# Optimization experiments

Hardware: AMD Instinct MI355X
Metric: run time of the kernel (lower is better)

Reference implementation:

```python
import jax, jax.numpy as jnp
import numpy as np

E, R, CIN, COUT = 8, 8, 256, 256
B, H, W = 16, 64, 64
DN = ('NCHW', 'OIHW', 'NCHW')


def setup_inputs() -> dict:
    key = jax.random.key(0)
    k1, k2, k3, k4 = jax.random.split(key, 4)
    x = jax.random.normal(k1, (B, CIN, H, W), jnp.float32)
    probs = jax.nn.softmax(jax.random.normal(k2, (E,), jnp.float32))
    # in conv: rank filters over in_channels, kernel (1,3); out conv: kernel (3,1)
    weight_in = jax.random.normal(k3, (E, R, CIN, 1, 3), jnp.float32) * 0.02
    weight_out = jax.random.normal(k4, (E, COUT, R, 3, 1), jnp.float32) * 0.02
    return {"x": x, "probs": probs, "weight_in": weight_in, "weight_out": weight_out}


def _expert_conv(x, w_in, w_out):
    # in conv: stride (1,1), padding (0,1) -> [B,R,H,W]
    h = jax.lax.conv_general_dilated(x, w_in, window_strides=(1, 1),
                                     padding=[(0, 0), (1, 1)], dimension_numbers=DN)
    # out conv: stride (1,1), padding (1,0) -> [B,COUT,H,W]
    return jax.lax.conv_general_dilated(h, w_out, window_strides=(1, 1),
                                        padding=[(1, 1), (0, 0)], dimension_numbers=DN)


def reference(x, probs, weight_in, weight_out):
    # vmap over experts replaces the Python loop; outs: [E,B,COUT,H,W]
    outs = jax.vmap(lambda wi, wo: _expert_conv(x, wi, wo))(weight_in, weight_out)
    # probability-weighted sum over experts (stack + sum in the original)
    return jnp.einsum('e,ebchw->bchw', probs, outs)
```

## Files before the change

### kernel.cpp

```cpp
#include <hip/hip_runtime.h>
#include <hip/hip_bf16.h>


typedef __bf16 bf16x8 __attribute__((ext_vector_type(8)));
typedef __bf16 bf16x4 __attribute__((ext_vector_type(4)));
typedef float  f32x4  __attribute__((ext_vector_type(4)));

#define CIN_  256
#define COUT_ 256
#define M1    64
#define K1    768
#define K2    192
#define CS    264
#define HS2   264

static __device__ __forceinline__ unsigned short f2bf(float f) {
    union { float f; unsigned u; } v; v.f = f;
    unsigned r = v.u + 0x7FFFu + ((v.u >> 16) & 1u);
    return (unsigned short)(r >> 16);
}

__global__ void prep_weights(const float* __restrict__ probs,
                             const float* __restrict__ w_in,
                             const float* __restrict__ w_out,
                             unsigned short* __restrict__ W1,
                             unsigned short* __restrict__ W2) {
    int idx = blockIdx.x * blockDim.x + threadIdx.x;
    if (idx < M1 * K1) {
        int er = idx / K1, rem = idx % K1;
        int kx = rem / CIN_, c = rem % CIN_;
        int e = er >> 3;
        W1[idx] = f2bf(probs[e] * w_in[(er * CIN_ + c) * 3 + kx]);
    } else {
        int i2 = idx - M1 * K1;
        int o = i2 / K2, rem = i2 % K2;
        int ky = rem / M1, er = rem % M1;
        int e = er >> 3, r = er & 7;
        W2[i2] = f2bf(w_out[((e * COUT_ + o) * 8 + r) * 3 + ky]);
    }
}

__global__ __launch_bounds__(256, 2)
void fused_kernel(const float* __restrict__ x,
                  const unsigned short* __restrict__ W1,
                  const unsigned short* __restrict__ W2,
                  float* __restrict__ out) {
    __shared__ unsigned short xs[66 * CS];
    __shared__ unsigned short hs[64 * HS2];
    const int bid  = blockIdx.x;
    const int b    = (bid & 7) + ((bid >> 8) << 3);
    const int s    = (bid >> 3) & 31;
    const int y0   = s << 1;
    const int tid  = threadIdx.x;
    const int lane = tid & 63;
    const int wave = tid >> 6;
    const int g    = lane >> 4;
    const int lr   = lane & 15;

    bf16x8 w1f[3][8];
    {
        const unsigned short* w1p = W1 + (wave * 16 + lr) * K1 + g * 8;
        #pragma unroll
        for (int kx = 0; kx < 3; ++kx)
            #pragma unroll
            for (int cc = 0; cc < 8; ++cc)
                w1f[kx][cc] = *(const bf16x8*)(w1p + kx * CIN_ + cc * 32);
    }

    if (tid < 66) {
        int row = (tid < 33) ? 0 : 65;
        int col = (tid - (tid < 33 ? 0 : 33)) * 8;
        bf16x4 z4 = {};
        *(bf16x4*)&xs[row * CS + col] = z4;
        *(bf16x4*)&xs[row * CS + col + 4] = z4;
    }

    const int crow = tid >> 4;
    const int n4   = (tid & 15) << 2;
    const int swzt = (tid & 7) << 3;

    for (int yy = 0; yy < 4; ++yy) {
        const int y = y0 - 1 + yy;
        const bool yok = ((unsigned)y < 64u);
        __syncthreads();
        const float* xbase = x + ((b * CIN_ + crow) * 64 + (yok ? y : 0)) * 64 + n4;
        unsigned short* wr = &xs[(n4 + 1) * CS];
        #pragma unroll
        for (int r = 0; r < 4; ++r) {
            float4 ld[4];
            if (yok) {
                #pragma unroll
                for (int q = 0; q < 4; ++q)
                    ld[q] = *(const float4*)(xbase + (r * 4 + q) * 16 * 4096);
            } else {
                #pragma unroll
                for (int q = 0; q < 4; ++q) ld[q] = make_float4(0.f, 0.f, 0.f, 0.f);
            }
            #pragma unroll
            for (int q = 0; q < 4; ++q) {
                int cx = ((r * 4 + q) * 16 + crow) ^ swzt;
                *(__bf16*)&wr[0 * CS + cx] = (__bf16)ld[q].x;
                *(__bf16*)&wr[1 * CS + cx] = (__bf16)ld[q].y;
                *(__bf16*)&wr[2 * CS + cx] = (__bf16)ld[q].z;
                *(__bf16*)&wr[3 * CS + cx] = (__bf16)ld[q].w;
            }
        }
        __syncthreads();

        f32x4 acc[4];
        #pragma unroll
        for (int i = 0; i < 4; ++i) acc[i] = (f32x4){0.f, 0.f, 0.f, 0.f};
        #pragma unroll
        for (int kx = 0; kx < 3; ++kx) {
            int ns0 = lr + kx;
            int sz0 = (((ns0 - 1) >> 2) & 7) << 3;
            int ns1 = ns0 + 16, sz1 = (((ns1 - 1) >> 2) & 7) << 3;
            int ns2 = ns0 + 32, sz2 = (((ns2 - 1) >> 2) & 7) << 3;
            int ns3 = ns0 + 48, sz3 = (((ns3 - 1) >> 2) & 7) << 3;
            const unsigned short* r0  = &xs[ns0 * CS];
            const unsigned short* r1  = &xs[ns1 * CS];
            const unsigned short* r2p = &xs[ns2 * CS];
            const unsigned short* r3  = &xs[ns3 * CS];
            #pragma unroll
            for (int cc = 0; cc < 8; ++cc) {
                int co = cc * 32 + g * 8;
                acc[0] = __builtin_amdgcn_mfma_f32_16x16x32_bf16(
                    w1f[kx][cc], *(const bf16x8*)&r0[co ^ sz0], acc[0], 0, 0, 0);
                acc[1] = __builtin_amdgcn_mfma_f32_16x16x32_bf16(
                    w1f[kx][cc], *(const bf16x8*)&r1[co ^ sz1], acc[1], 0, 0, 0);
                acc[2] = __builtin_amdgcn_mfma_f32_16x16x32_bf16(
                    w1f[kx][cc], *(const bf16x8*)&r2p[co ^ sz2], acc[2], 0, 0, 0);
                acc[3] = __builtin_amdgcn_mfma_f32_16x16x32_bf16(
                    w1f[kx][cc], *(const bf16x8*)&r3[co ^ sz3], acc[3], 0, 0, 0);
            }
        }
        #pragma unroll
        for (int nt = 0; nt < 4; ++nt) {
            int n = nt * 16 + lr;
            bf16x4 pk;
            #pragma unroll
            for (int r2 = 0; r2 < 4; ++r2) pk[r2] = (__bf16)acc[nt][r2];
            int col = (yy * 64 + wave * 16 + g * 4) ^ ((n & 7) << 3);
            *(bf16x4*)&hs[n * HS2 + col] = pk;
        }
    }
    __syncthreads();

    bf16x8 w2f[4][6];
    #pragma unroll
    for (int ot = 0; ot < 4; ++ot)
        #pragma unroll
        for (int kc = 0; kc < 6; ++kc)
            w2f[ot][kc] = *(const bf16x8*)(W2 + ((wave * 4 + ot) * 16 + lr) * K2 +
                                           kc * 32 + g * 8);

    #pragma unroll
    for (int ry = 0; ry < 2; ++ry) {
        f32x4 acc2[4][4];
        #pragma unroll
        for (int ot = 0; ot < 4; ++ot)
            #pragma unroll
            for (int nt = 0; nt < 4; ++nt) acc2[ot][nt] = (f32x4){0.f, 0.f, 0.f, 0.f};

        #pragma unroll
        for (int kc = 0; kc < 6; ++kc) {
            bf16x8 bfrag[4];
            #pragma unroll
            for (int nt = 0; nt < 4; ++nt) {
                int n = nt * 16 + lr;
                int col = (ry * 64 + kc * 32 + g * 8) ^ ((n & 7) << 3);
                bfrag[nt] = *(const bf16x8*)&hs[n * HS2 + col];
            }
            #pragma unroll
            for (int ot = 0; ot < 4; ++ot)
                #pragma unroll
                for (int nt = 0; nt < 4; ++nt)
                    acc2[ot][nt] = __builtin_amdgcn_mfma_f32_16x16x32_bf16(
                        w2f[ot][kc], bfrag[nt], acc2[ot][nt], 0, 0, 0);
        }

        const int yo = y0 + ry;
        #pragma unroll
        for (int ot = 0; ot < 4; ++ot) {
            #pragma unroll
            for (int r2 = 0; r2 < 4; ++r2) {
                int o = (wave * 4 + ot) * 16 + g * 4 + r2;
                float* orow = out + ((b * COUT_ + o) * 64 + yo) * 64;
                #pragma unroll
                for (int nt = 0; nt < 4; ++nt)
                    orow[nt * 16 + lr] = acc2[ot][nt][r2];
            }
        }
    }
}

extern "C" void kernel_launch(void* const* d_in, const int* in_sizes, int n_in,
                              void* d_out, int out_size, void* d_ws, size_t ws_size,
                              hipStream_t stream) {
    const float* x     = (const float*)d_in[0];
    const float* probs = (const float*)d_in[1];
    const float* w_in  = (const float*)d_in[2];
    const float* w_out = (const float*)d_in[3];
    float* out = (float*)d_out;

    unsigned short* W1 = (unsigned short*)d_ws;
    unsigned short* W2 = W1 + M1 * K1;

    prep_weights<<<384, 256, 0, stream>>>(probs, w_in, w_out, W1, W2);
    fused_kernel<<<16 * 32, 256, 0, stream>>>(x, W1, W2, out);
}
```

Baseline: 47.79 us.

## Use 512-thread blocks computing four output rows to cut halo recomputation

Each block now produces four output rows instead of two and runs 8 waves. The 8 waves split the first-stage GEMM by rank tile and half of the width. Six input rows are staged per block instead of four, so the redundant halo work on input rows and stage-1 recomputation falls from 2x to 1.5x, and the grid is halved to 256 blocks. The cost is a larger LDS hidden buffer, fewer blocks (256 on a 256-CU part, so roughly one block per CU), and less latency hiding from multiple resident blocks.

Result: slower. 50.92 us (+6.5%).

```diff
diff --git a/kernel.cpp b/kernel.cpp
--- a/kernel.cpp
+++ b/kernel.cpp
@@ -12,7 +12,7 @@
 #define K1    768
 #define K2    192
 #define CS    264
-#define HS2   264
+#define HSS   392
 
 static __device__ __forceinline__ unsigned short f2bf(float f) {
     union { float f; unsigned u; } v; v.f = f;
@@ -40,26 +40,28 @@
     }
 }
 
-__global__ __launch_bounds__(256, 2)
+__global__ __launch_bounds__(512)
 void fused_kernel(const float* __restrict__ x,
                   const unsigned short* __restrict__ W1,
                   const unsigned short* __restrict__ W2,
                   float* __restrict__ out) {
     __shared__ unsigned short xs[66 * CS];
-    __shared__ unsigned short hs[64 * HS2];
+    __shared__ unsigned short hs[64 * HSS];
     const int bid  = blockIdx.x;
-    const int b    = (bid & 7) + ((bid >> 8) << 3);
-    const int s    = (bid >> 3) & 31;
-    const int y0   = s << 1;
+    const int b    = (bid & 7) + ((bid >> 7) << 3);
+    const int s    = (bid >> 3) & 15;
+    const int y0   = s << 2;
     const int tid  = threadIdx.x;
     const int lane = tid & 63;
     const int wave = tid >> 6;
     const int g    = lane >> 4;
     const int lr   = lane & 15;
+    const int mt   = wave & 3;
+    const int nh   = wave >> 2;
 
     bf16x8 w1f[3][8];
     {
-        const unsigned short* w1p = W1 + (wave * 16 + lr) * K1 + g * 8;
+        const unsigned short* w1p = W1 + (mt * 16 + lr) * K1 + g * 8;
         #pragma unroll
         for (int kx = 0; kx < 3; ++kx)
             #pragma unroll
@@ -79,26 +81,26 @@
     const int n4   = (tid & 15) << 2;
     const int swzt = (tid & 7) << 3;
 
-    for (int yy = 0; yy < 4; ++yy) {
+    for (int yy = 0; yy < 6; ++yy) {
         const int y = y0 - 1 + yy;
         const bool yok = ((unsigned)y < 64u);
         __syncthreads();
         const float* xbase = x + ((b * CIN_ + crow) * 64 + (yok ? y : 0)) * 64 + n4;
         unsigned short* wr = &xs[(n4 + 1) * CS];
         #pragma unroll
-        for (int r = 0; r < 4; ++r) {
+        for (int r = 0; r < 2; ++r) {
             float4 ld[4];
             if (yok) {
                 #pragma unroll
                 for (int q = 0; q < 4; ++q)
-                    ld[q] = *(const float4*)(xbase + (r * 4 + q) * 16 * 4096);
+                    ld[q] = *(const float4*)(xbase + (r * 4 + q) * 32 * 4096);
             } else {
                 #pragma unroll
                 for (int q = 0; q < 4; ++q) ld[q] = make_float4(0.f, 0.f, 0.f, 0.f);
             }
             #pragma unroll
             for (int q = 0; q < 4; ++q) {
-                int cx = ((r * 4 + q) * 16 + crow) ^ swzt;
+                int cx = ((r * 4 + q) * 32 + crow) ^ swzt;
                 *(__bf16*)&wr[0 * CS + cx] = (__bf16)ld[q].x;
                 *(__bf16*)&wr[1 * CS + cx] = (__bf16)ld[q].y;
                 *(__bf16*)&wr[2 * CS + cx] = (__bf16)ld[q].z;
@@ -107,58 +109,51 @@
         }
         __syncthreads();
 
-        f32x4 acc[4];
-        #pragma unroll
-        for (int i = 0; i < 4; ++i) acc[i] = (f32x4){0.f, 0.f, 0.f, 0.f};
+        f32x4 acc[2];
+        acc[0] = (f32x4){0.f, 0.f, 0.f, 0.f};
+        acc[1] = (f32x4){0.f, 0.f, 0.f, 0.f};
         #pragma unroll
         for (int kx = 0; kx < 3; ++kx) {
-            int ns0 = lr + kx;
-            int sz0 = (((ns0 - 1) >> 2) & 7) << 3;
-            int ns1 = ns0 + 16, sz1 = (((ns1 - 1) >> 2) & 7) << 3;
-            int ns2 = ns0 + 32, sz2 = (((ns2 - 1) >> 2) & 7) << 3;
-            int ns3 = ns0 + 48, sz3 = (((ns3 - 1) >> 2) & 7) << 3;
-            const unsigned short* r0  = &xs[ns0 * CS];
-            const unsigned short* r1  = &xs[ns1 * CS];
-            const unsigned short* r2p = &xs[ns2 * CS];
-            const unsigned short* r3  = &xs[ns3 * CS];
+            int nA = nh * 32 + lr + kx - 1;
+            int nB = nA + 16;
+            int szA = ((nA >> 2) & 7) << 3;
+            int szB = ((nB >> 2) & 7) << 3;
+            const unsigned short* rA = &xs[(nA + 1) * CS];
+            const unsigned short* rB = &xs[(nB + 1) * CS];
             #pragma unroll
             for (int cc = 0; cc < 8; ++cc) {
                 int co = cc * 32 + g * 8;
                 acc[0] = __builtin_amdgcn_mfma_f32_16x16x32_bf16(
-                    w1f[kx][cc], *(const bf16x8*)&r0[co ^ sz0], acc[0], 0, 0, 0);
+                    w1f[kx][cc], *(const bf16x8*)&rA[co ^ szA], acc[0], 0, 0, 0);
                 acc[1] = __builtin_amdgcn_mfma_f32_16x16x32_bf16(
-                    w1f[kx][cc], *(const bf16x8*)&r1[co ^ sz1], acc[1], 0, 0, 0);
-                acc[2] = __builtin_amdgcn_mfma_f32_16x16x32_bf16(
-                    w1f[kx][cc], *(const bf16x8*)&r2p[co ^ sz2], acc[2], 0, 0, 0);
-                acc[3] = __builtin_amdgcn_mfma_f32_16x16x32_bf16(
-                    w1f[kx][cc], *(const bf16x8*)&r3[co ^ sz3], acc[3], 0, 0, 0);
-            }
-        }
-        #pragma unroll
-        for (int nt = 0; nt < 4; ++nt) {
-            int n = nt * 16 + lr;
+                    w1f[kx][cc], *(const bf16x8*)&rB[co ^ szB], acc[1], 0, 0, 0);
+            }
+        }
+        #pragma unroll
+        for (int nt = 0; nt < 2; ++nt) {
+            int n = nh * 32 + nt * 16 + lr;
             bf16x4 pk;
             #pragma unroll
             for (int r2 = 0; r2 < 4; ++r2) pk[r2] = (__bf16)acc[nt][r2];
-            int col = (yy * 64 + wave * 16 + g * 4) ^ ((n & 7) << 3);
-            *(bf16x4*)&hs[n * HS2 + col] = pk;
+            int col = (yy * 64 + mt * 16 + g * 4) ^ ((n & 7) << 3);
+            *(bf16x4*)&hs[n * HSS + col] = pk;
         }
     }
     __syncthreads();
 
-    bf16x8 w2f[4][6];
+    bf16x8 w2f[2][6];
     #pragma unroll
-    for (int ot = 0; ot < 4; ++ot)
+    for (int ot = 0; ot < 2; ++ot)
         #pragma unroll
         for (int kc = 0; kc < 6; ++kc)
-            w2f[ot][kc] = *(const bf16x8*)(W2 + ((wave * 4 + ot) * 16 + lr) * K2 +
+            w2f[ot][kc] = *(const bf16x8*)(W2 + ((wave * 2 + ot) * 16 + lr) * K2 +
                                            kc * 32 + g * 8);
 
     #pragma unroll
-    for (int ry = 0; ry < 2; ++ry) {
-        f32x4 acc2[4][4];
-        #pragma unroll
-        for (int ot = 0; ot < 4; ++ot)
+    for (int ry = 0; ry < 4; ++ry) {
+        f32x4 acc2[2][4];
+        #pragma unroll
+        for (int ot = 0; ot < 2; ++ot)
             #pragma unroll
             for (int nt = 0; nt < 4; ++nt) acc2[ot][nt] = (f32x4){0.f, 0.f, 0.f, 0.f};
 
@@ -169,10 +164,10 @@
             for (int nt = 0; nt < 4; ++nt) {
                 int n = nt * 16 + lr;
                 int col = (ry * 64 + kc * 32 + g * 8) ^ ((n & 7) << 3);
-                bfrag[nt] = *(const bf16x8*)&hs[n * HS2 + col];
-            }
-            #pragma unroll
-            for (int ot = 0; ot < 4; ++ot)
+                bfrag[nt] = *(const bf16x8*)&hs[n * HSS + col];
+            }
+            #pragma unroll
+            for (int ot = 0; ot < 2; ++ot)
                 #pragma unroll
                 for (int nt = 0; nt < 4; ++nt)
                     acc2[ot][nt] = __builtin_amdgcn_mfma_f32_16x16x32_bf16(
@@ -181,10 +176,10 @@
 
         const int yo = y0 + ry;
         #pragma unroll
-        for (int ot = 0; ot < 4; ++ot) {
+        for (int ot = 0; ot < 2; ++ot) {
             #pragma unroll
             for (int r2 = 0; r2 < 4; ++r2) {
-                int o = (wave * 4 + ot) * 16 + g * 4 + r2;
+                int o = (wave * 2 + ot) * 16 + g * 4 + r2;
                 float* orow = out + ((b * COUT_ + o) * 64 + yo) * 64;
                 #pragma unroll
                 for (int nt = 0; nt < 4; ++nt)
@@ -207,5 +202,5 @@
     unsigned short* W2 = W1 + M1 * K1;
 
     prep_weights<<<384, 256, 0, stream>>>(probs, w_in, w_out, W1, W2);
-    fused_kernel<<<16 * 32, 256, 0, stream>>>(x, W1, W2, out);
-}
+    fused_kernel<<<16 * 16, 512, 0, stream>>>(x, W1, W2, out);
+}
```
